# Optimization experiments

Hardware: AMD Instinct MI355X
Metric: run time of the kernel (lower is better)

The kernel has to match this reference:

```python
import math
import jax, jax.numpy as jnp
import numpy as np

NUM_HEADS = 16
EPS = 1e-6


def _rotate_half(t):
    t1, t2 = jnp.split(t, 2, axis=-1)
    return jnp.concatenate([-t2, t1], axis=-1)


def _rmsnorm(t, w):
    # compute in fp32 like the torch module, then cast back and apply affine
    x32 = t.astype(jnp.float32)
    r = jax.lax.rsqrt(jnp.mean(x32 * x32, axis=-1, keepdims=True) + EPS)
    return (x32 * r).astype(t.dtype) * w


def setup_inputs() -> dict:
    key = jax.random.key(0)
    ks = jax.random.split(key, 12)
    B, N, C, T = 8, 1024, 1024, 1024
    hd2 = (C // NUM_HEADS) // 2  # 32
    inp = {
        "x": jax.random.normal(ks[0], (B, N, C), jnp.float32),
        "temb": jax.random.normal(ks[1], (B, T), jnp.float32),
        "cos_y": jax.random.uniform(ks[2], (1, 1, N, hd2), jnp.float32, -1.0, 1.0),
        "sin_y": jax.random.uniform(ks[3], (1, 1, N, hd2), jnp.float32, -1.0, 1.0),
        "cos_x": jax.random.uniform(ks[4], (1, 1, N, hd2), jnp.float32, -1.0, 1.0),
        "sin_x": jax.random.uniform(ks[5], (1, 1, N, hd2), jnp.float32, -1.0, 1.0),
        # params; weights stored (in, out) so y = x @ W + b (== torch x @ W.T)
        "Wqkv": jax.random.normal(ks[6], (C, 3 * C), jnp.float32) * 0.02,
        "bqkv": jnp.zeros((3 * C,), jnp.float32),
        "Wt": jax.random.normal(ks[7], (T, 3 * C), jnp.float32) * 0.02,
        "bt": jnp.zeros((3 * C,), jnp.float32),
        "Wp": jax.random.normal(ks[8], (C, C), jnp.float32) * 0.02,
        "bp": jnp.zeros((C,), jnp.float32),
        "qn_w": jnp.ones((C // NUM_HEADS,), jnp.float32),
        "kn_w": jnp.ones((C // NUM_HEADS,), jnp.float32),
    }
    return inp


def reference(x, temb, cos_y, sin_y, cos_x, sin_x,
              Wqkv, bqkv, Wt, bt, Wp, bp, qn_w, kn_w):
    B, N, C = x.shape
    H = NUM_HEADS
    hd = C // H
    # fused QKV projection + additive time conditioning
    qkv = x @ Wqkv + bqkv + (temb @ Wt + bt)[:, None, :]         # [B,N,3C]
    qkv = qkv.reshape(B, N, 3, H, hd).transpose(2, 0, 3, 1, 4)    # [3,B,H,N,hd]
    q, k, v = qkv[0], qkv[1], qkv[2]
    # per-head QK RMSNorm with affine
    q = _rmsnorm(q, qn_w)
    k = _rmsnorm(k, kn_w)
    # axial 2D RoPE on the y-half and x-half of head_dim
    qy, qx = jnp.split(q, 2, axis=-1)
    ky, kx = jnp.split(k, 2, axis=-1)
    qy = qy * cos_y + _rotate_half(qy) * sin_y
    ky = ky * cos_y + _rotate_half(ky) * sin_y
    qx = qx * cos_x + _rotate_half(qx) * sin_x
    kx = kx * cos_x + _rotate_half(kx) * sin_x
    q = jnp.concatenate([qy, qx], axis=-1)
    k = jnp.concatenate([ky, kx], axis=-1)
    # scaled dot-product attention (no dropout at eval)
    scale = 1.0 / math.sqrt(hd)
    scores = jnp.einsum('bhqd,bhkd->bhqk', q, k) * scale
    attn = jax.nn.softmax(scores, axis=-1)
    out = jnp.einsum('bhqk,bhkd->bhqd', attn, v)                  # [B,H,N,hd]
    out = out.transpose(0, 2, 1, 3).reshape(B, N, C)
    return out @ Wp + bp
```

## Files before the change

### kernel.cpp

```cpp
#include <hip/hip_runtime.h>
#include <cstdint>

typedef unsigned short u16;
typedef __bf16 bf16x8 __attribute__((ext_vector_type(8)));
typedef float f32x4 __attribute__((ext_vector_type(4)));

__device__ __forceinline__ u16 f2bf(float f) {
  __bf16 h = (__bf16)f;
  return __builtin_bit_cast(u16, h);
}
__device__ __forceinline__ float bf2f(u16 u) {
  union { uint32_t u; float f; } v; v.u = ((uint32_t)u) << 16;
  return v.f;
}

__device__ __forceinline__ void gload16(const void* g, const void* l) {
  __builtin_amdgcn_global_load_lds(
      (const __attribute__((address_space(1))) uint32_t*)(uintptr_t)g,
      (__attribute__((address_space(3))) uint32_t*)(uintptr_t)l, 16, 0, 0);
}

__device__ __forceinline__ f32x4 mfma16(bf16x8 a, bf16x8 b, f32x4 c) {
  return __builtin_amdgcn_mfma_f32_16x16x32_bf16(a, b, c, 0, 0, 0);
}

__device__ __forceinline__ int swz(int row, int col) {
  return row * 64 + ((((col >> 3) ^ (row & 7)) << 3) | (col & 7));
}

__device__ __forceinline__ void transpose64(const float* __restrict__ src,
                                            u16* __restrict__ dst, int R, int Cc,
                                            int r0, int c0, u16* t) {
  #pragma unroll
  for (int i = 0; i < 16; i++) {
    int e = i * 256 + threadIdx.x;
    int rl = e >> 6, cl = e & 63;
    t[cl * 66 + rl] = f2bf(src[(size_t)(r0 + rl) * Cc + c0 + cl]);
  }
  __syncthreads();
  #pragma unroll
  for (int i = 0; i < 16; i++) {
    int e = i * 256 + threadIdx.x;
    int ro = e >> 6, co = e & 63;
    dst[(size_t)(c0 + ro) * R + r0 + co] = t[ro * 66 + co];
  }
}

__global__ __launch_bounds__(256)
void k_prep(const float* __restrict__ x, u16* __restrict__ x_bf,
            const float* __restrict__ Wqkv, u16* __restrict__ WqkvT,
            const float* __restrict__ Wp, u16* __restrict__ WpT,
            const float* __restrict__ temb, const float* __restrict__ Wt,
            float* __restrict__ tpart) {
  __shared__ u16 t[64 * 66];
  int bid = blockIdx.x;
  if (bid < 8192) {
    int i = bid * 256 + threadIdx.x;
    float4 v = ((const float4*)x)[i];
    union { u16 s[4]; uint2 u; } o;
    o.s[0] = f2bf(v.x); o.s[1] = f2bf(v.y); o.s[2] = f2bf(v.z); o.s[3] = f2bf(v.w);
    ((uint2*)x_bf)[i] = o.u;
    return;
  }
  bid -= 8192;
  if (bid < 768) {
    transpose64(Wqkv, WqkvT, 1024, 3072, (bid / 48) * 64, (bid % 48) * 64, t);
    return;
  }
  bid -= 768;
  if (bid < 256) {
    transpose64(Wp, WpT, 1024, 1024, (bid / 16) * 64, (bid % 16) * 64, t);
    return;
  }
  bid -= 256;
  {
    const int j = (bid % 12) * 256 + threadIdx.x;
    const int k0 = (bid / 12) * 32;
    float acc[8];
    #pragma unroll
    for (int b = 0; b < 8; b++) acc[b] = 0.f;
    #pragma unroll 4
    for (int k = k0; k < k0 + 32; k++) {
      float wv = Wt[(size_t)k * 3072 + j];
      #pragma unroll
      for (int b = 0; b < 8; b++) acc[b] += temb[b * 1024 + k] * wv;
    }
    float* p = tpart + (size_t)(bid / 12) * 24576 + j;
    #pragma unroll
    for (int b = 0; b < 8; b++) p[b * 3072] = acc[b];
  }
}

__global__ __launch_bounds__(256, 2)
void k_gemm0(const u16* __restrict__ A, const u16* __restrict__ Bt,
             u16* __restrict__ outb,
             const float* __restrict__ bt, const float* __restrict__ bqkv,
             const float* __restrict__ tpart, int K, int Ntot) {
  __shared__ u16 As[2][8192];
  __shared__ u16 Bs[2][4096];
  __shared__ float tcs[128];
  const int m0 = blockIdx.y * 256;
  const int n0 = blockIdx.x * 128;
  const int lane = threadIdx.x & 63;
  const int w = threadIdx.x >> 6;
  const int l15 = lane & 15;
  const int fo = (((lane >> 4) ^ ((lane >> 1) & 3)) << 3);
  const int srow = lane >> 2;
  const int schunk = (((lane & 3) ^ ((lane >> 3) & 3)) << 3);

  if (threadIdx.x < 128) {
    const int bidx = m0 >> 10;
    const int j = n0 + (int)threadIdx.x;
    float a = bt[j] + bqkv[j];
    #pragma unroll
    for (int kt = 0; kt < 32; kt++) a += tpart[(size_t)kt * 24576 + bidx * 3072 + j];
    tcs[threadIdx.x] = a;
  }
  asm volatile("" ::: "memory");

  f32x4 acc[4][8];
  #pragma unroll
  for (int i = 0; i < 4; i++)
    #pragma unroll
    for (int j = 0; j < 8; j++) acc[i][j] = (f32x4){0.f, 0.f, 0.f, 0.f};

  const u16* Ag = A + (size_t)(m0 + srow) * K + schunk;
  const u16* Bg = Bt + (size_t)(n0 + srow) * K + schunk;

  const int iters = K >> 5;
  #pragma unroll
  for (int tt = 0; tt < 4; tt++) {
    int t = w * 4 + tt;
    gload16(Ag + (size_t)(16 * t) * K, &As[0][t * 512]);
  }
  #pragma unroll
  for (int tt = 0; tt < 2; tt++) {
    int t = w * 2 + tt;
    gload16(Bg + (size_t)(16 * t) * K, &Bs[0][t * 512]);
  }

  for (int it = 0; it < iters; it++) {
    __syncthreads();
    const int cur = it & 1;
    if (it + 1 < iters) {
      const int nxt = cur ^ 1;
      const int k1 = (it + 1) << 5;
      #pragma unroll
      for (int tt = 0; tt < 4; tt++) {
        int t = w * 4 + tt;
        gload16(Ag + (size_t)(16 * t) * K + k1, &As[nxt][t * 512]);
      }
      #pragma unroll
      for (int tt = 0; tt < 2; tt++) {
        int t = w * 2 + tt;
        gload16(Bg + (size_t)(16 * t) * K + k1, &Bs[nxt][t * 512]);
      }
    }
    bf16x8 af[4], bfr[8];
    #pragma unroll
    for (int i = 0; i < 4; i++)
      af[i] = *(const bf16x8*)&As[cur][(w * 64 + 16 * i + l15) * 32 + fo];
    #pragma unroll
    for (int j = 0; j < 8; j++)
      bfr[j] = *(const bf16x8*)&Bs[cur][(16 * j + l15) * 32 + fo];
    #pragma unroll
    for (int i = 0; i < 4; i++)
      #pragma unroll
      for (int j = 0; j < 8; j++)
        acc[i][j] = mfma16(af[i], bfr[j], acc[i][j]);
  }

  const int rl = (lane >> 4) * 4;
  #pragma unroll
  for (int i = 0; i < 4; i++) {
    #pragma unroll
    for (int j = 0; j < 8; j++) {
      #pragma unroll
      for (int r = 0; r < 4; r++) {
        int grow = m0 + w * 64 + 16 * i + rl + r;
        int gcol = n0 + 16 * j + l15;
        float v = acc[i][j][r] + tcs[16 * j + l15];
        outb[(size_t)grow * Ntot + gcol] = f2bf(v);
      }
    }
  }
}

__global__ __launch_bounds__(512, 2)
void k_gemm1(const u16* __restrict__ A, const u16* __restrict__ Bt,
             float* __restrict__ outf, const float* __restrict__ bias,
             int K, int Ntot) {
  __shared__ __align__(16) u16 As[3][128 * 64];
  __shared__ __align__(16) u16 Bs[3][256 * 64];

  const int nb = (int)gridDim.x;
  const int bid = (int)blockIdx.x;
  const int sb = (bid & 7) * (nb >> 3) + (bid >> 3);
  const int NBN = Ntot >> 8;
  const int m0 = (sb / NBN) * 128;
  const int n0 = (sb % NBN) * 256;

  const int lane = threadIdx.x & 63;
  const int w = threadIdx.x >> 6;
  const int wm = w >> 2;
  const int wn = w & 3;
  const int l15 = lane & 15;
  const int g8 = (lane >> 4) * 8;
  const int lr = lane >> 3;
  const int schunk = ((lane & 7) ^ lr) * 8;

  const u16* Ag = A + (size_t)(m0 + w * 16 + lr) * K + schunk;
  const u16* Bg = Bt + (size_t)(n0 + lr) * K + schunk;

  f32x4 acc[4][4];
  #pragma unroll
  for (int i = 0; i < 4; i++)
    #pragma unroll
    for (int j = 0; j < 4; j++) acc[i][j] = (f32x4){0.f, 0.f, 0.f, 0.f};

  auto stageA_Blo = [&](int kt_, int buf_) {
    const int ko = kt_ << 6;
    #pragma unroll
    for (int t = 0; t < 2; t++) {
      int r0 = w * 16 + t * 8;
      gload16(Ag + (size_t)(t * 8) * K + ko, &As[buf_][r0 * 64]);
    }
    #pragma unroll
    for (int t = 0; t < 2; t++) {
      int f0 = w * 16 + t * 8;
      int r0 = (f0 >> 5) * 64 + (f0 & 31);
      gload16(Bg + (size_t)r0 * K + ko, &Bs[buf_][r0 * 64]);
    }
  };
  auto stageBhi = [&](int kt_, int buf_) {
    const int ko = kt_ << 6;
    #pragma unroll
    for (int t = 0; t < 2; t++) {
      int f0 = w * 16 + t * 8;
      int r0 = (f0 >> 5) * 64 + 32 + (f0 & 31);
      gload16(Bg + (size_t)r0 * K + ko, &Bs[buf_][r0 * 64]);
    }
  };

  const int NT = K >> 6;
  stageA_Blo(0, 0); stageBhi(0, 0);
  stageA_Blo(1, 1); stageBhi(1, 1);
  asm volatile("s_waitcnt vmcnt(8)" ::: "memory");
  __builtin_amdgcn_s_barrier();
  asm volatile("" ::: "memory");

  int cur = 0;
  for (int kt = 0; kt < NT; kt++) {
    const int nxtbuf = cur + 2 >= 3 ? cur - 1 : cur + 2;

    bf16x8 af[2][4], bfr[2][4];
    #pragma unroll
    for (int s = 0; s < 2; s++)
      #pragma unroll
      for (int mf = 0; mf < 4; mf++)
        af[s][mf] = *(const bf16x8*)&As[cur][swz(wm * 64 + mf * 16 + l15, s * 32 + g8)];
    #pragma unroll
    for (int s = 0; s < 2; s++)
      #pragma unroll
      for (int nf = 0; nf < 2; nf++)
        bfr[s][nf] = *(const bf16x8*)&Bs[cur][swz(wn * 64 + nf * 16 + l15, s * 32 + g8)];
    if (kt + 2 < NT) stageA_Blo(kt + 2, nxtbuf);
    if (kt <= NT - 2) asm volatile("s_waitcnt vmcnt(6)" ::: "memory");
    else              asm volatile("s_waitcnt vmcnt(0)" ::: "memory");
    __builtin_amdgcn_s_barrier();
    asm volatile("" ::: "memory");
    __builtin_amdgcn_s_setprio(1);
    #pragma unroll
    for (int s = 0; s < 2; s++)
      #pragma unroll
      for (int mf = 0; mf < 4; mf++)
        #pragma unroll
        for (int nf = 0; nf < 2; nf++)
          acc[mf][nf] = mfma16(af[s][mf], bfr[s][nf], acc[mf][nf]);
    __builtin_amdgcn_s_setprio(0);

    #pragma unroll
    for (int s = 0; s < 2; s++)
      #pragma unroll
      for (int nf = 2; nf < 4; nf++)
        bfr[s][nf] = *(const bf16x8*)&Bs[cur][swz(wn * 64 + nf * 16 + l15, s * 32 + g8)];
    if (kt + 2 < NT) stageBhi(kt + 2, nxtbuf);
    if (kt < NT - 2)       asm volatile("s_waitcnt vmcnt(6)" ::: "memory");
    else if (kt == NT - 2) asm volatile("s_waitcnt vmcnt(2)" ::: "memory");
    else                   asm volatile("s_waitcnt vmcnt(0)" ::: "memory");
    __builtin_amdgcn_s_barrier();
    asm volatile("" ::: "memory");
    __builtin_amdgcn_s_setprio(1);
    #pragma unroll
    for (int s = 0; s < 2; s++)
      #pragma unroll
      for (int mf = 0; mf < 4; mf++)
        #pragma unroll
        for (int nf = 2; nf < 4; nf++)
          acc[mf][nf] = mfma16(af[s][mf], bfr[s][nf], acc[mf][nf]);
    __builtin_amdgcn_s_setprio(0);

    cur = cur + 1 >= 3 ? 0 : cur + 1;
  }

  const int rl = (lane >> 4) * 4;
  #pragma unroll
  for (int mf = 0; mf < 4; mf++) {
    #pragma unroll
    for (int nf = 0; nf < 4; nf++) {
      #pragma unroll
      for (int r = 0; r < 4; r++) {
        int grow = m0 + wm * 64 + mf * 16 + rl + r;
        int gcol = n0 + wn * 64 + nf * 16 + l15;
        outf[(size_t)grow * Ntot + gcol] = acc[mf][nf][r] + bias[gcol];
      }
    }
  }
}

__global__ __launch_bounds__(256)
void k_rrv(const u16* __restrict__ qkv,
           const float* __restrict__ cos_y, const float* __restrict__ sin_y,
           const float* __restrict__ cos_x, const float* __restrict__ sin_x,
           const float* __restrict__ qn_w, const float* __restrict__ kn_w,
           u16* __restrict__ Qo, u16* __restrict__ Ko, u16* __restrict__ VT) {
  __shared__ u16 t[64 * 68];
  const int n0 = blockIdx.x * 64, h = blockIdx.y, b = blockIdx.z;
  const int bh = b * 16 + h;
  const int lane = threadIdx.x & 63, w = threadIdx.x >> 6;
  const int l15 = lane & 15, lg = lane >> 4;
  float4 qw = *(const float4*)(qn_w + l15 * 4);
  float4 kw = *(const float4*)(kn_w + l15 * 4);
  const float sgn = (lane & 4) ? 1.0f : -1.0f;
  const float* ct = (lane & 8) ? cos_x : cos_y;
  const float* st = (lane & 8) ? sin_x : sin_y;
  const float QSCALE = 0.18033688011112042f;

  #pragma unroll
  for (int rr = 0; rr < 4; rr++) {
    int row = n0 + w * 16 + rr * 4 + lg;
    size_t src = (size_t)(b * 1024 + row) * 3072 + h * 64 + l15 * 4;
    uint2 qu = *(const uint2*)(qkv + src);
    uint2 ku = *(const uint2*)(qkv + src + 1024);
    float q[4], k[4];
    q[0] = bf2f((u16)qu.x); q[1] = bf2f((u16)(qu.x >> 16));
    q[2] = bf2f((u16)qu.y); q[3] = bf2f((u16)(qu.y >> 16));
    k[0] = bf2f((u16)ku.x); k[1] = bf2f((u16)(ku.x >> 16));
    k[2] = bf2f((u16)ku.y); k[3] = bf2f((u16)(ku.y >> 16));
    float sq = q[0]*q[0] + q[1]*q[1] + q[2]*q[2] + q[3]*q[3];
    float sk = k[0]*k[0] + k[1]*k[1] + k[2]*k[2] + k[3]*k[3];
    #pragma unroll
    for (int m = 1; m < 16; m <<= 1) {
      sq += __shfl_xor(sq, m);
      sk += __shfl_xor(sk, m);
    }
    float rq = rsqrtf(sq * (1.0f / 64.0f) + 1e-6f);
    float rk = rsqrtf(sk * (1.0f / 64.0f) + 1e-6f);
    float4 cc = *(const float4*)(ct + (size_t)row * 32 + (lane & 7) * 4);
    float4 ss = *(const float4*)(st + (size_t)row * 32 + (lane & 7) * 4);
    float qn[4], kn[4];
    qn[0] = q[0]*rq*qw.x; qn[1] = q[1]*rq*qw.y; qn[2] = q[2]*rq*qw.z; qn[3] = q[3]*rq*qw.w;
    kn[0] = k[0]*rk*kw.x; kn[1] = k[1]*rk*kw.y; kn[2] = k[2]*rk*kw.z; kn[3] = k[3]*rk*kw.w;
    float c[4] = {cc.x, cc.y, cc.z, cc.w};
    float s[4] = {ss.x, ss.y, ss.z, ss.w};
    union { u16 e[4]; uint2 u; } oq, ok;
    #pragma unroll
    for (int j = 0; j < 4; j++) {
      float qp = __shfl_xor(qn[j], 4);
      float kp = __shfl_xor(kn[j], 4);
      oq.e[j] = f2bf((qn[j] * c[j] + sgn * qp * s[j]) * QSCALE);
      ok.e[j] = f2bf(kn[j] * c[j] + sgn * kp * s[j]);
    }
    size_t dst = ((size_t)bh * 1024 + row) * 64 + l15 * 4;
    *(uint2*)(Qo + dst) = oq.u;
    *(uint2*)(Ko + dst) = ok.u;
  }

  #pragma unroll
  for (int i = 0; i < 4; i++) {
    int e = i * 256 + threadIdx.x;
    int n = e >> 4, dc = e & 15;
    uint2 v = *(const uint2*)(qkv + (size_t)(b * 1024 + n0 + n) * 3072 + 2048 + h * 64 + dc * 4);
    t[(dc * 4 + 0) * 68 + n] = (u16)v.x;
    t[(dc * 4 + 1) * 68 + n] = (u16)(v.x >> 16);
    t[(dc * 4 + 2) * 68 + n] = (u16)v.y;
    t[(dc * 4 + 3) * 68 + n] = (u16)(v.y >> 16);
  }
  __syncthreads();
  #pragma unroll
  for (int i = 0; i < 4; i++) {
    int e = i * 256 + threadIdx.x;
    int d = e >> 4, nc = e & 15;
    const u16* p = &t[d * 68 + nc * 4];
    uint2 o;
    o.x = (uint32_t)p[0] | ((uint32_t)p[1] << 16);
    o.y = (uint32_t)p[2] | ((uint32_t)p[3] << 16);
    *(uint2*)(VT + ((size_t)bh * 64 + d) * 1024 + n0 + nc * 4) = o;
  }
}

__global__ __launch_bounds__(256, 2)
void k_attn(const u16* __restrict__ Q, const u16* __restrict__ Kb,
            const u16* __restrict__ VT, u16* __restrict__ Ob) {
  __shared__ u16 Ks[2][4096], VTs[2][4096];
  const int lane = threadIdx.x & 63;
  const int w = threadIdx.x >> 6;
  const int bh = blockIdx.x;
  const int qt = blockIdx.y;
  const int b = bh >> 4, h = bh & 15;
  const size_t base = (size_t)bh * 65536;
  const int q0 = qt * 128;
  const int scol = ((lane & 7) ^ (lane >> 3)) * 8;
  const int lr = lane >> 3;
  const int l15 = lane & 15;
  const int g = lane >> 4;

  bf16x8 aq[2][2];
  #pragma unroll
  for (int i = 0; i < 2; i++)
    #pragma unroll
    for (int s = 0; s < 2; s++)
      aq[i][s] = *(const bf16x8*)(Q + base +
          (size_t)(q0 + w * 32 + i * 16 + l15) * 64 + s * 32 + g * 8);

  f32x4 acc_o[2][4];
  float lpar[2] = {0.f, 0.f};
  #pragma unroll
  for (int i = 0; i < 2; i++)
    #pragma unroll
    for (int dt = 0; dt < 4; dt++) acc_o[i][dt] = (f32x4){0.f, 0.f, 0.f, 0.f};

  #pragma unroll
  for (int tt = 0; tt < 2; tt++) {
    int t = w * 2 + tt;
    gload16(Kb + base + (size_t)(8 * t + lr) * 64 + scol, &Ks[0][t * 512]);
    gload16(VT + base + (size_t)(8 * t + lr) * 1024 + scol, &VTs[0][t * 512]);
  }

  for (int it = 0; it < 16; it++) {
    __syncthreads();
    const int cur = it & 1;
    if (it < 15) {
      const int nxt = cur ^ 1;
      const int j1 = (it + 1) * 64;
      #pragma unroll
      for (int tt = 0; tt < 2; tt++) {
        int t = w * 2 + tt;
        gload16(Kb + base + (size_t)(j1 + 8 * t + lr) * 64 + scol, &Ks[nxt][t * 512]);
        gload16(VT + base + (size_t)(8 * t + lr) * 1024 + j1 + scol, &VTs[nxt][t * 512]);
      }
    }
    const u16* K_ = Ks[cur];
    const u16* V_ = VTs[cur];

    f32x4 accs[2][4];
    #pragma unroll
    for (int i = 0; i < 2; i++)
      #pragma unroll
      for (int nt = 0; nt < 4; nt++) accs[i][nt] = (f32x4){0.f, 0.f, 0.f, 0.f};
    #pragma unroll
    for (int s = 0; s < 2; s++) {
      bf16x8 bk[4];
      #pragma unroll
      for (int nt = 0; nt < 4; nt++)
        bk[nt] = *(const bf16x8*)&K_[swz(nt * 16 + l15, s * 32 + g * 8)];
      __builtin_amdgcn_s_setprio(1);
      #pragma unroll
      for (int i = 0; i < 2; i++)
        #pragma unroll
        for (int nt = 0; nt < 4; nt++)
          accs[i][nt] = mfma16(bk[nt], aq[i][s], accs[i][nt]);
      __builtin_amdgcn_s_setprio(0);
    }

    float p[2][4][4];
    #pragma unroll
    for (int i = 0; i < 2; i++)
      #pragma unroll
      for (int nt = 0; nt < 4; nt++)
        #pragma unroll
        for (int r = 0; r < 4; r++) {
          p[i][nt][r] = __builtin_amdgcn_exp2f(accs[i][nt][r]);
          lpar[i] += p[i][nt][r];
        }

    #pragma unroll
    for (int s = 0; s < 2; s++) {
      union { uint32_t u[4]; bf16x8 v; } ap[2];
      #pragma unroll
      for (int i = 0; i < 2; i++)
        #pragma unroll
        for (int m = 0; m < 4; m++)
          asm("v_cvt_pk_bf16_f32 %0, %1, %2"
              : "=v"(ap[i].u[m])
              : "v"(p[i][2 * s + (m >> 1)][2 * (m & 1)]),
                "v"(p[i][2 * s + (m >> 1)][2 * (m & 1) + 1]));
      bf16x8 bv[4];
      #pragma unroll
      for (int dt = 0; dt < 4; dt++) {
        union { uint2 x2[2]; bf16x8 v; } bb;
        bb.x2[0] = *(const uint2*)&V_[swz(dt * 16 + l15, s * 32 + 4 * g)];
        bb.x2[1] = *(const uint2*)&V_[swz(dt * 16 + l15, s * 32 + 16 + 4 * g)];
        bv[dt] = bb.v;
      }
      __builtin_amdgcn_s_setprio(1);
      #pragma unroll
      for (int dt = 0; dt < 4; dt++) {
        acc_o[0][dt] = mfma16(ap[0].v, bv[dt], acc_o[0][dt]);
        acc_o[1][dt] = mfma16(ap[1].v, bv[dt], acc_o[1][dt]);
      }
      __builtin_amdgcn_s_setprio(0);
    }
  }

  #pragma unroll
  for (int i = 0; i < 2; i++) {
    float lred = lpar[i];
    lred += __shfl_xor(lred, 16);
    lred += __shfl_xor(lred, 32);
    float inv[4];
    #pragma unroll
    for (int r = 0; r < 4; r++) {
      float lv = __shfl(lred, 4 * g + r);
      inv[r] = 1.0f / lv;
    }
    #pragma unroll
    for (int dt = 0; dt < 4; dt++)
      #pragma unroll
      for (int r = 0; r < 4; r++) {
        int row = q0 + w * 32 + i * 16 + 4 * g + r;
        int col = h * 64 + dt * 16 + l15;
        Ob[((size_t)b * 1024 + row) * 1024 + col] = f2bf(acc_o[i][dt][r] * inv[r]);
      }
  }
}

extern "C" void kernel_launch(void* const* d_in, const int* in_sizes, int n_in,
                              void* d_out, int out_size, void* d_ws, size_t ws_size,
                              hipStream_t stream) {
  const float* x     = (const float*)d_in[0];
  const float* temb  = (const float*)d_in[1];
  const float* cos_y = (const float*)d_in[2];
  const float* sin_y = (const float*)d_in[3];
  const float* cos_x = (const float*)d_in[4];
  const float* sin_x = (const float*)d_in[5];
  const float* Wqkv  = (const float*)d_in[6];
  const float* bqkv  = (const float*)d_in[7];
  const float* Wt    = (const float*)d_in[8];
  const float* bt    = (const float*)d_in[9];
  const float* Wp    = (const float*)d_in[10];
  const float* bp    = (const float*)d_in[11];
  const float* qn_w  = (const float*)d_in[12];
  const float* kn_w  = (const float*)d_in[13];
  float* out = (float*)d_out;

  char* ws = (char*)d_ws;
  u16*   x_bf  = (u16*)(ws);
  u16*   WqkvT = (u16*)(ws + 16777216);
  u16*   WpT   = (u16*)(ws + 23068672);
  u16*   qkv   = (u16*)(ws + 25264128);
  u16*   Qb    = (u16*)(ws + 75595776);
  u16*   Kb    = (u16*)(ws + 92372992);
  u16*   VTb   = (u16*)(ws + 109150208);
  float* tpart = (float*)(ws + 125927424);
  u16*   att   = x_bf;

  k_prep<<<9600, 256, 0, stream>>>(x, x_bf, Wqkv, WqkvT, Wp, WpT, temb, Wt, tpart);
  k_gemm0<<<dim3(24, 32), 256, 0, stream>>>(x_bf, WqkvT, qkv, bt, bqkv, tpart,
                                            1024, 3072);
  k_rrv<<<dim3(16, 16, 8), 256, 0, stream>>>(qkv, cos_y, sin_y, cos_x, sin_x,
                                             qn_w, kn_w, Qb, Kb, VTb);
  k_attn<<<dim3(128, 8), 256, 0, stream>>>(Qb, Kb, VTb, att);
  k_gemm1<<<dim3(256), 512, 0, stream>>>(att, WpT, out, bp, 1024, 1024);
}
```

Before: 269.5 us.

## Widen attention blocks to 256 queries and swizzle QKV GEMM block order

The attention kernel now runs 512 threads per block covering 256 query rows, so each K/V tile staged in LDS is shared by eight waves instead of four. Only the first four waves issue the loads. The exp/convert step is interleaved per half-tile to cut live registers. The QKV GEMM moves to a 1D grid with an XCD-aware block remapping (bid&7 spread), meant to improve L2 locality on the multi-die GPU. Risks include fewer attention blocks (512) for the CU count and register pressure under the 512-thread launch bound.

```diff
diff --git a/kernel.cpp b/kernel.cpp
--- a/kernel.cpp
+++ b/kernel.cpp
@@ -99,8 +99,12 @@
   __shared__ u16 As[2][8192];
   __shared__ u16 Bs[2][4096];
   __shared__ float tcs[128];
-  const int m0 = blockIdx.y * 256;
-  const int n0 = blockIdx.x * 128;
+  const int nb = (int)gridDim.x;
+  const int bid = (int)blockIdx.x;
+  const int sb = (bid & 7) * (nb >> 3) + (bid >> 3);
+  const int NBN = Ntot >> 7;
+  const int m0 = (sb / NBN) * 256;
+  const int n0 = (sb % NBN) * 128;
   const int lane = threadIdx.x & 63;
   const int w = threadIdx.x >> 6;
   const int l15 = lane & 15;
@@ -399,7 +403,7 @@
   }
 }
 
-__global__ __launch_bounds__(256, 2)
+__global__ __launch_bounds__(512, 2)
 void k_attn(const u16* __restrict__ Q, const u16* __restrict__ Kb,
             const u16* __restrict__ VT, u16* __restrict__ Ob) {
   __shared__ u16 Ks[2][4096], VTs[2][4096];
@@ -409,7 +413,7 @@
   const int qt = blockIdx.y;
   const int b = bh >> 4, h = bh & 15;
   const size_t base = (size_t)bh * 65536;
-  const int q0 = qt * 128;
+  const int q0 = qt * 256 + w * 32;
   const int scol = ((lane & 7) ^ (lane >> 3)) * 8;
   const int lr = lane >> 3;
   const int l15 = lane & 15;
@@ -421,7 +425,7 @@
     #pragma unroll
     for (int s = 0; s < 2; s++)
       aq[i][s] = *(const bf16x8*)(Q + base +
-          (size_t)(q0 + w * 32 + i * 16 + l15) * 64 + s * 32 + g * 8);
+          (size_t)(q0 + i * 16 + l15) * 64 + s * 32 + g * 8);
 
   f32x4 acc_o[2][4];
   float lpar[2] = {0.f, 0.f};
@@ -430,17 +434,19 @@
     #pragma unroll
     for (int dt = 0; dt < 4; dt++) acc_o[i][dt] = (f32x4){0.f, 0.f, 0.f, 0.f};
 
-  #pragma unroll
-  for (int tt = 0; tt < 2; tt++) {
-    int t = w * 2 + tt;
-    gload16(Kb + base + (size_t)(8 * t + lr) * 64 + scol, &Ks[0][t * 512]);
-    gload16(VT + base + (size_t)(8 * t + lr) * 1024 + scol, &VTs[0][t * 512]);
+  if (w < 4) {
+    #pragma unroll
+    for (int tt = 0; tt < 2; tt++) {
+      int t = w * 2 + tt;
+      gload16(Kb + base + (size_t)(8 * t + lr) * 64 + scol, &Ks[0][t * 512]);
+      gload16(VT + base + (size_t)(8 * t + lr) * 1024 + scol, &VTs[0][t * 512]);
+    }
   }
 
   for (int it = 0; it < 16; it++) {
     __syncthreads();
     const int cur = it & 1;
-    if (it < 15) {
+    if (w < 4 && it < 15) {
       const int nxt = cur ^ 1;
       const int j1 = (it + 1) * 64;
       #pragma unroll
@@ -473,19 +479,18 @@
       __builtin_amdgcn_s_setprio(0);
     }
 
-    float p[2][4][4];
-    #pragma unroll
-    for (int i = 0; i < 2; i++)
-      #pragma unroll
-      for (int nt = 0; nt < 4; nt++)
+    #pragma unroll
+    for (int s = 0; s < 2; s++) {
+      float pv[2][2][4];
+      #pragma unroll
+      for (int i = 0; i < 2; i++)
         #pragma unroll
-        for (int r = 0; r < 4; r++) {
-          p[i][nt][r] = __builtin_amdgcn_exp2f(accs[i][nt][r]);
-          lpar[i] += p[i][nt][r];
-        }
-
-    #pragma unroll
-    for (int s = 0; s < 2; s++) {
+        for (int th = 0; th < 2; th++)
+          #pragma unroll
+          for (int r = 0; r < 4; r++) {
+            pv[i][th][r] = __builtin_amdgcn_exp2f(accs[i][2 * s + th][r]);
+            lpar[i] += pv[i][th][r];
+          }
       union { uint32_t u[4]; bf16x8 v; } ap[2];
       #pragma unroll
       for (int i = 0; i < 2; i++)
@@ -493,8 +498,8 @@
         for (int m = 0; m < 4; m++)
           asm("v_cvt_pk_bf16_f32 %0, %1, %2"
               : "=v"(ap[i].u[m])
-              : "v"(p[i][2 * s + (m >> 1)][2 * (m & 1)]),
-                "v"(p[i][2 * s + (m >> 1)][2 * (m & 1) + 1]));
+              : "v"(pv[i][m >> 1][2 * (m & 1)]),
+                "v"(pv[i][m >> 1][2 * (m & 1) + 1]));
       bf16x8 bv[4];
       #pragma unroll
       for (int dt = 0; dt < 4; dt++) {
@@ -528,7 +533,7 @@
     for (int dt = 0; dt < 4; dt++)
       #pragma unroll
       for (int r = 0; r < 4; r++) {
-        int row = q0 + w * 32 + i * 16 + 4 * g + r;
+        int row = q0 + i * 16 + 4 * g + r;
         int col = h * 64 + dt * 16 + l15;
         Ob[((size_t)b * 1024 + row) * 1024 + col] = f2bf(acc_o[i][dt][r] * inv[r]);
       }
@@ -566,10 +571,10 @@
   u16*   att   = x_bf;
 
   k_prep<<<9600, 256, 0, stream>>>(x, x_bf, Wqkv, WqkvT, Wp, WpT, temb, Wt, tpart);
-  k_gemm0<<<dim3(24, 32), 256, 0, stream>>>(x_bf, WqkvT, qkv, bt, bqkv, tpart,
-                                            1024, 3072);
+  k_gemm0<<<dim3(768), 256, 0, stream>>>(x_bf, WqkvT, qkv, bt, bqkv, tpart,
+                                         1024, 3072);
   k_rrv<<<dim3(16, 16, 8), 256, 0, stream>>>(qkv, cos_y, sin_y, cos_x, sin_x,
                                              qn_w, kn_w, Qb, Kb, VTb);
-  k_attn<<<dim3(128, 8), 256, 0, stream>>>(Qb, Kb, VTb, att);
+  k_attn<<<dim3(128, 4), 512, 0, stream>>>(Qb, Kb, VTb, att);
   k_gemm1<<<dim3(256), 512, 0, stream>>>(att, WpT, out, bp, 1024, 1024);
 }
```

Measured after the change: 272.7 us. About the same (+1.2%).

## Restructure QKV GEMM with 256x256 tiles, 4-stage pipeline, and swizzled block order

Applied to the files above, without the earlier changes.

The QKV projection GEMM moves from 256x128 tiles with 4 waves and double buffering to 256x256 tiles with 8 waves (2x4 wave grid). A 4-buffer LDS ring keeps three k-tiles of global loads in flight, using explicit vmcnt waits, split barriers and setprio around the MFMA bursts. Blocks are launched on a 1D grid with an XCD-style swizzle for L2 locality. The aim is more data reuse per tile and better overlap of loads with MFMA work. The cost is 128KB of LDS per block, which may limit occupancy, and fewer blocks (384).

```diff
diff --git a/kernel.cpp b/kernel.cpp
--- a/kernel.cpp
+++ b/kernel.cpp
@@ -91,24 +91,32 @@
   }
 }
 
-__global__ __launch_bounds__(256, 2)
+__global__ __launch_bounds__(512, 2)
 void k_gemm0(const u16* __restrict__ A, const u16* __restrict__ Bt,
              u16* __restrict__ outb,
              const float* __restrict__ bt, const float* __restrict__ bqkv,
              const float* __restrict__ tpart, int K, int Ntot) {
-  __shared__ u16 As[2][8192];
-  __shared__ u16 Bs[2][4096];
-  __shared__ float tcs[128];
-  const int m0 = blockIdx.y * 256;
-  const int n0 = blockIdx.x * 128;
+  __shared__ u16 As[4][8192];
+  __shared__ u16 Bs[4][8192];
+  __shared__ float tcs[256];
+
+  const int nb = (int)gridDim.x;
+  const int bid = (int)blockIdx.x;
+  const int sb = (bid & 7) * (nb >> 3) + (bid >> 3);
+  const int NBN = Ntot >> 8;
+  const int m0 = (sb / NBN) * 256;
+  const int n0 = (sb % NBN) * 256;
+
   const int lane = threadIdx.x & 63;
   const int w = threadIdx.x >> 6;
+  const int wm = w >> 2;
+  const int wn = w & 3;
   const int l15 = lane & 15;
   const int fo = (((lane >> 4) ^ ((lane >> 1) & 3)) << 3);
   const int srow = lane >> 2;
   const int schunk = (((lane & 3) ^ ((lane >> 3) & 3)) << 3);
 
-  if (threadIdx.x < 128) {
+  if (threadIdx.x < 256) {
     const int bidx = m0 >> 10;
     const int j = n0 + (int)threadIdx.x;
     float a = bt[j] + bqkv[j];
@@ -118,68 +126,85 @@
   }
   asm volatile("" ::: "memory");
 
-  f32x4 acc[4][8];
-  #pragma unroll
-  for (int i = 0; i < 4; i++)
-    #pragma unroll
-    for (int j = 0; j < 8; j++) acc[i][j] = (f32x4){0.f, 0.f, 0.f, 0.f};
+  f32x4 acc[8][4];
+  #pragma unroll
+  for (int i = 0; i < 8; i++)
+    #pragma unroll
+    for (int j = 0; j < 4; j++) acc[i][j] = (f32x4){0.f, 0.f, 0.f, 0.f};
 
   const u16* Ag = A + (size_t)(m0 + srow) * K + schunk;
   const u16* Bg = Bt + (size_t)(n0 + srow) * K + schunk;
 
-  const int iters = K >> 5;
-  #pragma unroll
-  for (int tt = 0; tt < 4; tt++) {
-    int t = w * 4 + tt;
-    gload16(Ag + (size_t)(16 * t) * K, &As[0][t * 512]);
-  }
-  #pragma unroll
-  for (int tt = 0; tt < 2; tt++) {
-    int t = w * 2 + tt;
-    gload16(Bg + (size_t)(16 * t) * K, &Bs[0][t * 512]);
-  }
-
-  for (int it = 0; it < iters; it++) {
-    __syncthreads();
-    const int cur = it & 1;
-    if (it + 1 < iters) {
-      const int nxt = cur ^ 1;
-      const int k1 = (it + 1) << 5;
-      #pragma unroll
-      for (int tt = 0; tt < 4; tt++) {
-        int t = w * 4 + tt;
-        gload16(Ag + (size_t)(16 * t) * K + k1, &As[nxt][t * 512]);
-      }
-      #pragma unroll
-      for (int tt = 0; tt < 2; tt++) {
-        int t = w * 2 + tt;
-        gload16(Bg + (size_t)(16 * t) * K + k1, &Bs[nxt][t * 512]);
-      }
-    }
-    bf16x8 af[4], bfr[8];
-    #pragma unroll
-    for (int i = 0; i < 4; i++)
-      af[i] = *(const bf16x8*)&As[cur][(w * 64 + 16 * i + l15) * 32 + fo];
-    #pragma unroll
-    for (int j = 0; j < 8; j++)
-      bfr[j] = *(const bf16x8*)&Bs[cur][(16 * j + l15) * 32 + fo];
-    #pragma unroll
-    for (int i = 0; i < 4; i++)
-      #pragma unroll
-      for (int j = 0; j < 8; j++)
-        acc[i][j] = mfma16(af[i], bfr[j], acc[i][j]);
+  auto stage = [&](int kt_, int buf_) {
+    const int ko = kt_ << 5;
+    #pragma unroll
+    for (int tt = 0; tt < 2; tt++) {
+      int t = w * 2 + tt;
+      gload16(Ag + (size_t)(16 * t) * K + ko, &As[buf_][t * 512]);
+    }
+    #pragma unroll
+    for (int tt = 0; tt < 2; tt++) {
+      int t = w * 2 + tt;
+      gload16(Bg + (size_t)(16 * t) * K + ko, &Bs[buf_][t * 512]);
+    }
+  };
+
+  const int NT = K >> 5;
+  stage(0, 0); stage(1, 1); stage(2, 2);
+  asm volatile("s_waitcnt vmcnt(8) lgkmcnt(0)" ::: "memory");
+  __builtin_amdgcn_s_barrier();
+  asm volatile("" ::: "memory");
+
+  for (int kt = 0; kt < NT; kt++) {
+    const u16* Ab = As[kt & 3];
+    const u16* Bb = Bs[kt & 3];
+
+    bf16x8 af[4], bfr[4];
+    #pragma unroll
+    for (int mf = 0; mf < 4; mf++)
+      af[mf] = *(const bf16x8*)&Ab[(wm * 128 + mf * 16 + l15) * 32 + fo];
+    #pragma unroll
+    for (int nf = 0; nf < 4; nf++)
+      bfr[nf] = *(const bf16x8*)&Bb[(wn * 64 + nf * 16 + l15) * 32 + fo];
+    __builtin_amdgcn_s_barrier();
+    asm volatile("" ::: "memory");
+    __builtin_amdgcn_s_setprio(1);
+    #pragma unroll
+    for (int mf = 0; mf < 4; mf++)
+      #pragma unroll
+      for (int nf = 0; nf < 4; nf++)
+        acc[mf][nf] = mfma16(af[mf], bfr[nf], acc[mf][nf]);
+    __builtin_amdgcn_s_setprio(0);
+
+    bf16x8 ah[4];
+    #pragma unroll
+    for (int mf = 0; mf < 4; mf++)
+      ah[mf] = *(const bf16x8*)&Ab[(wm * 128 + 64 + mf * 16 + l15) * 32 + fo];
+    if (kt + 3 < NT) stage(kt + 3, (kt + 3) & 3);
+    if (kt <= NT - 4)      asm volatile("s_waitcnt vmcnt(8)" ::: "memory");
+    else if (kt == NT - 3) asm volatile("s_waitcnt vmcnt(4)" ::: "memory");
+    else if (kt == NT - 2) asm volatile("s_waitcnt vmcnt(0)" ::: "memory");
+    __builtin_amdgcn_s_barrier();
+    asm volatile("" ::: "memory");
+    __builtin_amdgcn_s_setprio(1);
+    #pragma unroll
+    for (int mf = 0; mf < 4; mf++)
+      #pragma unroll
+      for (int nf = 0; nf < 4; nf++)
+        acc[4 + mf][nf] = mfma16(ah[mf], bfr[nf], acc[4 + mf][nf]);
+    __builtin_amdgcn_s_setprio(0);
   }
 
   const int rl = (lane >> 4) * 4;
   #pragma unroll
-  for (int i = 0; i < 4; i++) {
-    #pragma unroll
-    for (int j = 0; j < 8; j++) {
+  for (int mf = 0; mf < 8; mf++) {
+    #pragma unroll
+    for (int nf = 0; nf < 4; nf++) {
       #pragma unroll
       for (int r = 0; r < 4; r++) {
-        int grow = m0 + w * 64 + 16 * i + rl + r;
-        int gcol = n0 + 16 * j + l15;
-        float v = acc[i][j][r] + tcs[16 * j + l15];
+        int grow = m0 + wm * 128 + mf * 16 + rl + r;
+        int gcol = n0 + wn * 64 + nf * 16 + l15;
+        float v = acc[mf][nf][r] + tcs[wn * 64 + nf * 16 + l15];
         outb[(size_t)grow * Ntot + gcol] = f2bf(v);
       }
     }
@@ -566,8 +591,8 @@
   u16*   att   = x_bf;
 
   k_prep<<<9600, 256, 0, stream>>>(x, x_bf, Wqkv, WqkvT, Wp, WpT, temb, Wt, tpart);
-  k_gemm0<<<dim3(24, 32), 256, 0, stream>>>(x_bf, WqkvT, qkv, bt, bqkv, tpart,
-                                            1024, 3072);
+  k_gemm0<<<dim3(384), 512, 0, stream>>>(x_bf, WqkvT, qkv, bt, bqkv, tpart,
+                                         1024, 3072);
   k_rrv<<<dim3(16, 16, 8), 256, 0, stream>>>(qkv, cos_y, sin_y, cos_x, sin_x,
                                              qn_w, kn_w, Qb, Kb, VTb);
   k_attn<<<dim3(128, 8), 256, 0, stream>>>(Qb, Kb, VTb, att);
```

New measurement: 276.9 us. 2.7% more time.

## Remap gemm0 blocks with XCD swizzle and simplify gemm1 to 128x128 double-buffered tiles

Applied to the files above, without the earlier changes.

gemm0 moves from a 2D grid to a 1D grid whose block IDs are remapped so that consecutive blocks on the same XCD share tiles, which should improve L2 reuse. gemm1 drops its 3-stage 128x256 pipeline with split B loads, manual vmcnt waits and setprio. In its place is a simpler 256-thread kernel that computes 128x128 tiles with K=32 double buffering and uses twice as many blocks. This gives more parallelism and occupancy, but it also means less reuse per block and more barriers for each unit of K.

```diff
diff --git a/kernel.cpp b/kernel.cpp
--- a/kernel.cpp
+++ b/kernel.cpp
@@ -99,8 +99,12 @@
   __shared__ u16 As[2][8192];
   __shared__ u16 Bs[2][4096];
   __shared__ float tcs[128];
-  const int m0 = blockIdx.y * 256;
-  const int n0 = blockIdx.x * 128;
+  const int nb = (int)gridDim.x;
+  const int bid = (int)blockIdx.x;
+  const int sb = (bid & 7) * (nb >> 3) + (bid >> 3);
+  const int NBN = Ntot >> 7;
+  const int m0 = (sb / NBN) * 256;
+  const int n0 = (sb % NBN) * 128;
   const int lane = threadIdx.x & 63;
   const int w = threadIdx.x >> 6;
   const int l15 = lane & 15;
@@ -186,133 +190,79 @@
   }
 }
 
-__global__ __launch_bounds__(512, 2)
+__global__ __launch_bounds__(256, 2)
 void k_gemm1(const u16* __restrict__ A, const u16* __restrict__ Bt,
              float* __restrict__ outf, const float* __restrict__ bias,
              int K, int Ntot) {
-  __shared__ __align__(16) u16 As[3][128 * 64];
-  __shared__ __align__(16) u16 Bs[3][256 * 64];
-
+  __shared__ u16 As[2][4096];
+  __shared__ u16 Bs[2][4096];
   const int nb = (int)gridDim.x;
   const int bid = (int)blockIdx.x;
   const int sb = (bid & 7) * (nb >> 3) + (bid >> 3);
-  const int NBN = Ntot >> 8;
+  const int NBN = Ntot >> 7;
   const int m0 = (sb / NBN) * 128;
-  const int n0 = (sb % NBN) * 256;
-
+  const int n0 = (sb % NBN) * 128;
   const int lane = threadIdx.x & 63;
   const int w = threadIdx.x >> 6;
-  const int wm = w >> 2;
-  const int wn = w & 3;
   const int l15 = lane & 15;
-  const int g8 = (lane >> 4) * 8;
-  const int lr = lane >> 3;
-  const int schunk = ((lane & 7) ^ lr) * 8;
-
-  const u16* Ag = A + (size_t)(m0 + w * 16 + lr) * K + schunk;
-  const u16* Bg = Bt + (size_t)(n0 + lr) * K + schunk;
-
-  f32x4 acc[4][4];
-  #pragma unroll
-  for (int i = 0; i < 4; i++)
-    #pragma unroll
-    for (int j = 0; j < 4; j++) acc[i][j] = (f32x4){0.f, 0.f, 0.f, 0.f};
-
-  auto stageA_Blo = [&](int kt_, int buf_) {
-    const int ko = kt_ << 6;
-    #pragma unroll
-    for (int t = 0; t < 2; t++) {
-      int r0 = w * 16 + t * 8;
-      gload16(Ag + (size_t)(t * 8) * K + ko, &As[buf_][r0 * 64]);
-    }
-    #pragma unroll
-    for (int t = 0; t < 2; t++) {
-      int f0 = w * 16 + t * 8;
-      int r0 = (f0 >> 5) * 64 + (f0 & 31);
-      gload16(Bg + (size_t)r0 * K + ko, &Bs[buf_][r0 * 64]);
-    }
-  };
-  auto stageBhi = [&](int kt_, int buf_) {
-    const int ko = kt_ << 6;
-    #pragma unroll
-    for (int t = 0; t < 2; t++) {
-      int f0 = w * 16 + t * 8;
-      int r0 = (f0 >> 5) * 64 + 32 + (f0 & 31);
-      gload16(Bg + (size_t)r0 * K + ko, &Bs[buf_][r0 * 64]);
-    }
-  };
-
-  const int NT = K >> 6;
-  stageA_Blo(0, 0); stageBhi(0, 0);
-  stageA_Blo(1, 1); stageBhi(1, 1);
-  asm volatile("s_waitcnt vmcnt(8)" ::: "memory");
-  __builtin_amdgcn_s_barrier();
-  asm volatile("" ::: "memory");
-
-  int cur = 0;
-  for (int kt = 0; kt < NT; kt++) {
-    const int nxtbuf = cur + 2 >= 3 ? cur - 1 : cur + 2;
-
-    bf16x8 af[2][4], bfr[2][4];
-    #pragma unroll
-    for (int s = 0; s < 2; s++)
-      #pragma unroll
-      for (int mf = 0; mf < 4; mf++)
-        af[s][mf] = *(const bf16x8*)&As[cur][swz(wm * 64 + mf * 16 + l15, s * 32 + g8)];
-    #pragma unroll
-    for (int s = 0; s < 2; s++)
-      #pragma unroll
-      for (int nf = 0; nf < 2; nf++)
-        bfr[s][nf] = *(const bf16x8*)&Bs[cur][swz(wn * 64 + nf * 16 + l15, s * 32 + g8)];
-    if (kt + 2 < NT) stageA_Blo(kt + 2, nxtbuf);
-    if (kt <= NT - 2) asm volatile("s_waitcnt vmcnt(6)" ::: "memory");
-    else              asm volatile("s_waitcnt vmcnt(0)" ::: "memory");
-    __builtin_amdgcn_s_barrier();
-    asm volatile("" ::: "memory");
-    __builtin_amdgcn_s_setprio(1);
-    #pragma unroll
-    for (int s = 0; s < 2; s++)
-      #pragma unroll
-      for (int mf = 0; mf < 4; mf++)
-        #pragma unroll
-        for (int nf = 0; nf < 2; nf++)
-          acc[mf][nf] = mfma16(af[s][mf], bfr[s][nf], acc[mf][nf]);
-    __builtin_amdgcn_s_setprio(0);
-
-    #pragma unroll
-    for (int s = 0; s < 2; s++)
-      #pragma unroll
-      for (int nf = 2; nf < 4; nf++)
-        bfr[s][nf] = *(const bf16x8*)&Bs[cur][swz(wn * 64 + nf * 16 + l15, s * 32 + g8)];
-    if (kt + 2 < NT) stageBhi(kt + 2, nxtbuf);
-    if (kt < NT - 2)       asm volatile("s_waitcnt vmcnt(6)" ::: "memory");
-    else if (kt == NT - 2) asm volatile("s_waitcnt vmcnt(2)" ::: "memory");
-    else                   asm volatile("s_waitcnt vmcnt(0)" ::: "memory");
-    __builtin_amdgcn_s_barrier();
-    asm volatile("" ::: "memory");
-    __builtin_amdgcn_s_setprio(1);
-    #pragma unroll
-    for (int s = 0; s < 2; s++)
-      #pragma unroll
-      for (int mf = 0; mf < 4; mf++)
-        #pragma unroll
-        for (int nf = 2; nf < 4; nf++)
-          acc[mf][nf] = mfma16(af[s][mf], bfr[s][nf], acc[mf][nf]);
-    __builtin_amdgcn_s_setprio(0);
-
-    cur = cur + 1 >= 3 ? 0 : cur + 1;
+  const int fo = (((lane >> 4) ^ ((lane >> 1) & 3)) << 3);
+  const int srow = lane >> 2;
+  const int schunk = (((lane & 3) ^ ((lane >> 3) & 3)) << 3);
+
+  f32x4 acc[2][8];
+  #pragma unroll
+  for (int i = 0; i < 2; i++)
+    #pragma unroll
+    for (int j = 0; j < 8; j++) acc[i][j] = (f32x4){0.f, 0.f, 0.f, 0.f};
+
+  const u16* Ag = A + (size_t)(m0 + srow) * K + schunk;
+  const u16* Bg = Bt + (size_t)(n0 + srow) * K + schunk;
+
+  const int iters = K >> 5;
+  #pragma unroll
+  for (int tt = 0; tt < 2; tt++) {
+    int t = w * 2 + tt;
+    gload16(Ag + (size_t)(16 * t) * K, &As[0][t * 512]);
+    gload16(Bg + (size_t)(16 * t) * K, &Bs[0][t * 512]);
+  }
+
+  for (int it = 0; it < iters; it++) {
+    __syncthreads();
+    const int cur = it & 1;
+    if (it + 1 < iters) {
+      const int nxt = cur ^ 1;
+      const int k1 = (it + 1) << 5;
+      #pragma unroll
+      for (int tt = 0; tt < 2; tt++) {
+        int t = w * 2 + tt;
+        gload16(Ag + (size_t)(16 * t) * K + k1, &As[nxt][t * 512]);
+        gload16(Bg + (size_t)(16 * t) * K + k1, &Bs[nxt][t * 512]);
+      }
+    }
+    bf16x8 af[2], bfr[8];
+    #pragma unroll
+    for (int i = 0; i < 2; i++)
+      af[i] = *(const bf16x8*)&As[cur][(w * 32 + 16 * i + l15) * 32 + fo];
+    #pragma unroll
+    for (int j = 0; j < 8; j++)
+      bfr[j] = *(const bf16x8*)&Bs[cur][(16 * j + l15) * 32 + fo];
+    #pragma unroll
+    for (int i = 0; i < 2; i++)
+      #pragma unroll
+      for (int j = 0; j < 8; j++)
+        acc[i][j] = mfma16(af[i], bfr[j], acc[i][j]);
   }
 
   const int rl = (lane >> 4) * 4;
   #pragma unroll
-  for (int mf = 0; mf < 4; mf++) {
-    #pragma unroll
-    for (int nf = 0; nf < 4; nf++) {
+  for (int i = 0; i < 2; i++) {
+    #pragma unroll
+    for (int j = 0; j < 8; j++) {
       #pragma unroll
       for (int r = 0; r < 4; r++) {
-        int grow = m0 + wm * 64 + mf * 16 + rl + r;
-        int gcol = n0 + wn * 64 + nf * 16 + l15;
-        outf[(size_t)grow * Ntot + gcol] = acc[mf][nf][r] + bias[gcol];
+        int grow = m0 + w * 32 + 16 * i + rl + r;
+        int gcol = n0 + 16 * j + l15;
+        outf[(size_t)grow * Ntot + gcol] = acc[i][j][r] + bias[gcol];
       }
     }
   }
@@ -566,10 +516,10 @@
   u16*   att   = x_bf;
 
   k_prep<<<9600, 256, 0, stream>>>(x, x_bf, Wqkv, WqkvT, Wp, WpT, temb, Wt, tpart);
-  k_gemm0<<<dim3(24, 32), 256, 0, stream>>>(x_bf, WqkvT, qkv, bt, bqkv, tpart,
-                                            1024, 3072);
+  k_gemm0<<<dim3(768), 256, 0, stream>>>(x_bf, WqkvT, qkv, bt, bqkv, tpart,
+                                         1024, 3072);
   k_rrv<<<dim3(16, 16, 8), 256, 0, stream>>>(qkv, cos_y, sin_y, cos_x, sin_x,
                                              qn_w, kn_w, Qb, Kb, VTb);
   k_attn<<<dim3(128, 8), 256, 0, stream>>>(Qb, Kb, VTb, att);
-  k_gemm1<<<dim3(256), 512, 0, stream>>>(att, WpT, out, bp, 1024, 1024);
-}
+  k_gemm1<<<dim3(512), 256, 0, stream>>>(att, WpT, out, bp, 1024, 1024);
+}
```

After: 279.3 us. +3.6%, slower.
